# Optimization experiments

Hardware: AMD Instinct MI355X
Metric: run time of the kernel (lower is better)

## Reference

```python
import jax, jax.numpy as jnp
import numpy as np

N_NODES = 50000
N_EDGES = 800000
H = 128            # node_hidden_size
T = 2              # num_prop_rounds


def setup_inputs() -> dict:
    key = jax.random.key(0)
    ks = jax.random.split(key, 10)
    hv = jax.random.normal(ks[0], (N_NODES, H), dtype=jnp.float32)
    he = jax.random.normal(ks[1], (N_EDGES, 1), dtype=jnp.float32)
    src = jax.random.randint(ks[2], (N_EDGES,), 0, N_NODES, dtype=jnp.int32)
    dst = jax.random.randint(ks[3], (N_EDGES,), 0, N_NODES, dtype=jnp.int32)
    # per-round params, stacked on leading T axis; small scale to avoid gate saturation
    W_msg = jax.random.normal(ks[4], (T, 2 * H, 2 * H + 1), dtype=jnp.float32) * 0.05
    b_msg = jax.random.normal(ks[5], (T, 2 * H), dtype=jnp.float32) * 0.05
    W_ih = jax.random.normal(ks[6], (T, 3 * H, 2 * H), dtype=jnp.float32) * 0.05
    W_hh = jax.random.normal(ks[7], (T, 3 * H, H), dtype=jnp.float32) * 0.05
    b_ih = jax.random.normal(ks[8], (T, 3 * H), dtype=jnp.float32) * 0.05
    b_hh = jax.random.normal(ks[9], (T, 3 * H), dtype=jnp.float32) * 0.05
    return dict(hv=hv, he=he, src=src, dst=dst, W_msg=W_msg, b_msg=b_msg,
                W_ih=W_ih, W_hh=W_hh, b_ih=b_ih, b_hh=b_hh)


def _gru_cell(x, h, W_ih, W_hh, b_ih, b_hh):
    # torch.nn.GRUCell math
    gi = x @ W_ih.T + b_ih          # [N, 3H]
    gh = h @ W_hh.T + b_hh          # [N, 3H]
    i_r, i_z, i_n = jnp.split(gi, 3, axis=1)
    h_r, h_z, h_n = jnp.split(gh, 3, axis=1)
    r = jax.nn.sigmoid(i_r + h_r)
    z = jax.nn.sigmoid(i_z + h_z)
    n = jnp.tanh(i_n + r * h_n)
    return (1.0 - z) * n + z * h


def reference(hv, he, src, dst, W_msg, b_msg, W_ih, W_hh, b_ih, b_hh):
    n_nodes = hv.shape[0]
    for t in range(T):
        # per-edge message input: concat([hv_dst, hv_src, he])  [E, 2H+1]
        msg_in = jnp.concatenate([hv[dst], hv[src], he], axis=1)
        edge_act = msg_in @ W_msg[t].T + b_msg[t]          # [E, 2H]
        # ragged sum-reduce over incoming edges (deg-0 nodes get zeros)
        a = jax.ops.segment_sum(edge_act, dst, num_segments=n_nodes)  # [N, 2H]
        hv = _gru_cell(a, hv, W_ih[t], W_hh[t], b_ih[t], b_hh[t])
    return hv
```

## Files before the change

kernel.cpp:

```cpp
#include <hip/hip_runtime.h>
#include <cstdint>
#include <cstddef>

#define N_NODES 50000
#define N_EDGES 800000
#define HDIM 128
#define TROUNDS 2
#define NTILES 3125
#define PACK_PER_T (416 * 64)
#define MAXDEG 64

typedef __attribute__((ext_vector_type(8))) _Float16 half8v;
typedef __attribute__((ext_vector_type(2))) _Float16 half2v;
typedef __attribute__((ext_vector_type(4))) float f32x4;
typedef unsigned short ushort_t;

#define GLD_LDS(gp, lp)                                                        \
  __builtin_amdgcn_global_load_lds(                                            \
      (__attribute__((address_space(1))) const void*)(gp),                     \
      (__attribute__((address_space(3))) void*)(lp), 16, 0, 0)

static __device__ __forceinline__ float sigmoidf_(float x) {
  return 1.0f / (1.0f + __expf(-x));
}
static __device__ __forceinline__ float tanhf_(float x) {
  float xc = fminf(15.0f, fmaxf(-15.0f, x));
  float a = __expf(2.0f * xc);
  return (a - 1.0f) / (a + 1.0f);
}
static __device__ __forceinline__ float f16bits2f(uint32_t hb) {
  ushort_t u = (ushort_t)hb;
  _Float16 h;
  __builtin_memcpy(&h, &u, 2);
  return (float)h;
}

__global__ void pack_all(const float* __restrict__ Wmsg, const float* __restrict__ Wih,
                         const float* __restrict__ Whh, _Float16* __restrict__ W1p,
                         _Float16* __restrict__ W2p, float* __restrict__ we) {
  int g = blockIdx.x * blockDim.x + threadIdx.x;
  if (g < TROUNDS * 256) {
    int t = g >> 8, j = g & 255;
    we[g] = Wmsg[((size_t)t * 256 + j) * 257 + 256];
  }
  if (g >= TROUNDS * PACK_PER_T) return;
  int t = g / PACK_PER_T;
  int r = g % PACK_PER_T;
  int lane = r & 63;
  int fr = r >> 6;
  const float* srcp;
  _Float16* dstp;
  if (fr < 128) {
    int jt = fr >> 3, kt = fr & 7;
    int j = jt * 16 + (lane & 15);
    int k = kt * 32 + ((lane >> 4) << 3);
    srcp = Wmsg + (size_t)t * 256 * 257 + (size_t)j * 257 + k;
    dstp = W1p + ((size_t)t * 128 + fr) * 512 + lane * 8;
  } else {
    int fr2 = fr - 128;
    int chunk = fr2 / 12, idx = fr2 % 12;
    int jt = chunk / 3, pp = chunk % 3;
    int j = pp * 128 + jt * 16 + (lane & 15);
    int k;
    if (idx < 8) {
      k = idx * 32 + ((lane >> 4) << 3);
      srcp = Wih + (size_t)t * 384 * 256 + (size_t)j * 256 + k;
    } else {
      k = (idx - 8) * 32 + ((lane >> 4) << 3);
      srcp = Whh + (size_t)t * 384 * 128 + (size_t)j * 128 + k;
    }
    dstp = W2p + ((size_t)t * 288 + fr2) * 512 + lane * 8;
  }
  #pragma unroll
  for (int e = 0; e < 8; ++e) dstp[e] = (_Float16)srcp[e];
}

__global__ void cast_hv(const float* __restrict__ hv, _Float16* __restrict__ hvh) {
  int i = blockIdx.x * blockDim.x + threadIdx.x;
  if (i >= N_NODES * HDIM / 4) return;
  float4 v = reinterpret_cast<const float4*>(hv)[i];
  half2v o0, o1;
  o0[0] = (_Float16)v.x; o0[1] = (_Float16)v.y;
  o1[0] = (_Float16)v.z; o1[1] = (_Float16)v.w;
  reinterpret_cast<half2v*>(hvh)[i * 2] = o0;
  reinterpret_cast<half2v*>(hvh)[i * 2 + 1] = o1;
}

__global__ void fill_pad(const int* __restrict__ src, const int* __restrict__ dst,
                         const float* __restrict__ he, int* __restrict__ cnt,
                         uint32_t* __restrict__ csr) {
  int e = blockIdx.x * blockDim.x + threadIdx.x;
  if (e >= N_EDGES) return;
  int d = dst[e];
  int slot = atomicAdd(&cnt[d], 1);
  if (slot < MAXDEG) {
    _Float16 hh = (_Float16)he[e];
    ushort_t hb;
    __builtin_memcpy(&hb, &hh, 2);
    uint32_t en = ((uint32_t)hb << 16) | (uint32_t)src[e];
    csr[(size_t)d * MAXDEG + slot] = en;
  }
}

__global__ void gather_h(const _Float16* __restrict__ hvh, const int* __restrict__ cnt,
                         const uint32_t* __restrict__ csr, _Float16* __restrict__ S_h,
                         float* __restrict__ hsum, float* __restrict__ deg_f, int n) {
  int wid = (int)((blockIdx.x * blockDim.x + threadIdx.x) >> 6);
  int lane = threadIdx.x & 63;
  if (wid >= n) return;
  int deg = min(cnt[wid], MAXDEG);
  uint32_t ent = (lane < deg) ? csr[(size_t)wid * MAXDEG + lane] : 0u;
  float a0 = 0.f, a1 = 0.f, hs = 0.f;
  int k = 0;
  for (; k + 3 < deg; k += 4) {
    uint32_t e0 = __shfl(ent, k), e1 = __shfl(ent, k + 1);
    uint32_t e2 = __shfl(ent, k + 2), e3 = __shfl(ent, k + 3);
    half2v v0 = *reinterpret_cast<const half2v*>(hvh + (size_t)(e0 & 0xffffu) * HDIM + lane * 2);
    half2v v1 = *reinterpret_cast<const half2v*>(hvh + (size_t)(e1 & 0xffffu) * HDIM + lane * 2);
    half2v v2 = *reinterpret_cast<const half2v*>(hvh + (size_t)(e2 & 0xffffu) * HDIM + lane * 2);
    half2v v3 = *reinterpret_cast<const half2v*>(hvh + (size_t)(e3 & 0xffffu) * HDIM + lane * 2);
    a0 += ((float)v0[0] + (float)v1[0]) + ((float)v2[0] + (float)v3[0]);
    a1 += ((float)v0[1] + (float)v1[1]) + ((float)v2[1] + (float)v3[1]);
    hs += (f16bits2f(e0 >> 16) + f16bits2f(e1 >> 16)) +
          (f16bits2f(e2 >> 16) + f16bits2f(e3 >> 16));
  }
  for (; k < deg; ++k) {
    uint32_t e0 = __shfl(ent, k);
    half2v v0 = *reinterpret_cast<const half2v*>(hvh + (size_t)(e0 & 0xffffu) * HDIM + lane * 2);
    a0 += (float)v0[0];
    a1 += (float)v0[1];
    hs += f16bits2f(e0 >> 16);
  }
  half2v o;
  o[0] = (_Float16)a0;
  o[1] = (_Float16)a1;
  *reinterpret_cast<half2v*>(S_h + (size_t)wid * HDIM + lane * 2) = o;
  if (lane == 0) hsum[wid] = hs;
  if (lane == 1) deg_f[wid] = (float)deg;
}

__global__ __launch_bounds__(256, 4) void u1_kernel(
    const float* __restrict__ hv, const _Float16* __restrict__ S_h,
    const float* __restrict__ deg_f, const float* __restrict__ hsum,
    const _Float16* __restrict__ W1p, const float* __restrict__ we,
    const float* __restrict__ bmsg, _Float16* __restrict__ a_out) {
  __shared__ _Float16 buf[2][8 * 512];
  const int tid = threadIdx.x;
  const int wv = tid >> 6, lane = tid & 63;
  const int tile = blockIdx.x * 4 + wv;
  const bool act = (tile < NTILES);
  const int rowA = tile * 16 + (lane & 15);
  const int koff = (lane >> 4) * 8;
  const int m0 = (lane >> 4) * 4;

  {
    const _Float16* g = W1p + (size_t)(wv * 2) * 512 + lane * 8;
    #pragma unroll
    for (int i = 0; i < 2; ++i) GLD_LDS(g + i * 512, &buf[0][(wv * 2 + i) * 512]);
  }

  half8v x[8];
  float degs[4], hss[4];
  if (act) {
    float deg = deg_f[rowA];
    const float* hrow = hv + (size_t)rowA * HDIM;
    #pragma unroll
    for (int kt = 0; kt < 4; ++kt) {
      const float* sp = hrow + kt * 32 + koff;
      #pragma unroll
      for (int e = 0; e < 8; ++e) x[kt][e] = (_Float16)(sp[e] * deg);
    }
    const _Float16* srow = S_h + (size_t)rowA * HDIM + koff;
    #pragma unroll
    for (int kt = 0; kt < 4; ++kt)
      x[4 + kt] = *reinterpret_cast<const half8v*>(srow + kt * 32);
    #pragma unroll
    for (int rr = 0; rr < 4; ++rr) {
      degs[rr] = deg_f[tile * 16 + m0 + rr];
      hss[rr] = hsum[tile * 16 + m0 + rr];
    }
  }

  #pragma unroll 1
  for (int jt = 0; jt < 16; ++jt) {
    __syncthreads();
    if (jt < 15) {
      const _Float16* g = W1p + (size_t)(jt + 1) * 4096 + (size_t)(wv * 2) * 512 + lane * 8;
      #pragma unroll
      for (int i = 0; i < 2; ++i) GLD_LDS(g + i * 512, &buf[(jt + 1) & 1][(wv * 2 + i) * 512]);
    }
    const _Float16* B = &buf[jt & 1][0];
    f32x4 acc = {0.f, 0.f, 0.f, 0.f};
    #pragma unroll
    for (int kt = 0; kt < 8; ++kt) {
      half8v b = *reinterpret_cast<const half8v*>(B + (size_t)kt * 512 + lane * 8);
      acc = __builtin_amdgcn_mfma_f32_16x16x32_f16(x[kt], b, acc, 0, 0, 0);
    }
    if (act) {
      int j = jt * 16 + (lane & 15);
      float bm = bmsg[j], w = we[j];
      #pragma unroll
      for (int rr = 0; rr < 4; ++rr)
        a_out[(size_t)(tile * 16 + m0 + rr) * 256 + j] =
            (_Float16)(acc[rr] + degs[rr] * bm + hss[rr] * w);
    }
  }
}

__global__ __launch_bounds__(256, 4) void u2_kernel(
    const float* __restrict__ hv_in, const _Float16* __restrict__ a_in,
    const _Float16* __restrict__ W2p, const float* __restrict__ bih,
    const float* __restrict__ bhh, float* __restrict__ hv_out,
    _Float16* __restrict__ hvh_out) {
  __shared__ _Float16 buf[2][12 * 512];
  const int tid = threadIdx.x;
  const int wv = tid >> 6, lane = tid & 63;
  const int tile = blockIdx.x * 4 + wv;
  const bool act = (tile < NTILES);
  const int rowA = tile * 16 + (lane & 15);
  const int koff = (lane >> 4) * 8;
  const int m0 = (lane >> 4) * 4;

  auto stage = [&](int n) {
    const _Float16* g = W2p + (size_t)n * 6144 + (size_t)(wv * 3) * 512 + lane * 8;
    _Float16* l = &buf[n & 1][(wv * 3) * 512];
    #pragma unroll
    for (int i = 0; i < 3; ++i) GLD_LDS(g + i * 512, l + i * 512);
  };

  stage(0);

  half8v a8[8], h4[4];
  if (act) {
    const _Float16* ar = a_in + (size_t)rowA * 256 + koff;
    #pragma unroll
    for (int kt = 0; kt < 8; ++kt)
      a8[kt] = *reinterpret_cast<const half8v*>(ar + kt * 32);
    const float* hr = hv_in + (size_t)rowA * HDIM + koff;
    #pragma unroll
    for (int kt = 0; kt < 4; ++kt) {
      #pragma unroll
      for (int e = 0; e < 8; ++e) h4[kt][e] = (_Float16)hr[kt * 32 + e];
    }
  }

  auto compute = [&](const _Float16* B, f32x4& ai, f32x4& ag) {
    ai = (f32x4){0.f, 0.f, 0.f, 0.f};
    ag = (f32x4){0.f, 0.f, 0.f, 0.f};
    #pragma unroll
    for (int kt = 0; kt < 8; ++kt) {
      half8v b = *reinterpret_cast<const half8v*>(B + (size_t)kt * 512 + lane * 8);
      ai = __builtin_amdgcn_mfma_f32_16x16x32_f16(a8[kt], b, ai, 0, 0, 0);
    }
    #pragma unroll
    for (int kt = 0; kt < 4; ++kt) {
      half8v b = *reinterpret_cast<const half8v*>(B + (size_t)(8 + kt) * 512 + lane * 8);
      ag = __builtin_amdgcn_mfma_f32_16x16x32_f16(h4[kt], b, ag, 0, 0, 0);
    }
  };

  f32x4 rreg, zreg, ai, ag;
  #pragma unroll 1
  for (int jt = 0; jt < 8; ++jt) {
    const int c0 = jt * 3;
    const int fcol = jt * 16 + (lane & 15);
    __syncthreads();
    stage(c0 + 1);
    compute(&buf[c0 & 1][0], ai, ag);
    if (act) {
      float bi = bih[fcol], bq = bhh[fcol];
      #pragma unroll
      for (int rr = 0; rr < 4; ++rr) rreg[rr] = sigmoidf_(ai[rr] + bi + ag[rr] + bq);
    }
    __syncthreads();
    stage(c0 + 2);
    compute(&buf[(c0 + 1) & 1][0], ai, ag);
    if (act) {
      float bi = bih[128 + fcol], bq = bhh[128 + fcol];
      #pragma unroll
      for (int rr = 0; rr < 4; ++rr) zreg[rr] = sigmoidf_(ai[rr] + bi + ag[rr] + bq);
    }
    __syncthreads();
    if (jt < 7) stage(c0 + 3);
    compute(&buf[(c0 + 2) & 1][0], ai, ag);
    if (act) {
      float bi = bih[256 + fcol], bq = bhh[256 + fcol];
      #pragma unroll
      for (int rr = 0; rr < 4; ++rr) {
        int node = tile * 16 + m0 + rr;
        float n = tanhf_(ai[rr] + bi + rreg[rr] * (ag[rr] + bq));
        float h = hv_in[(size_t)node * HDIM + fcol];
        float hn = (1.f - zreg[rr]) * n + zreg[rr] * h;
        hv_out[(size_t)node * HDIM + fcol] = hn;
        hvh_out[(size_t)node * HDIM + fcol] = (_Float16)hn;
      }
    }
  }
}

extern "C" void kernel_launch(void* const* d_in, const int* in_sizes, int n_in,
                              void* d_out, int out_size, void* d_ws, size_t ws_size,
                              hipStream_t stream) {
  const float* hv   = (const float*)d_in[0];
  const float* he   = (const float*)d_in[1];
  const int*   src  = (const int*)d_in[2];
  const int*   dst  = (const int*)d_in[3];
  const float* Wmsg = (const float*)d_in[4];
  const float* bmsg = (const float*)d_in[5];
  const float* Wih  = (const float*)d_in[6];
  const float* Whh  = (const float*)d_in[7];
  const float* bih  = (const float*)d_in[8];
  const float* bhh  = (const float*)d_in[9];

  char* p = (char*)d_ws;
  auto alloc = [&](size_t bytes) { char* r = p; p += (bytes + 255) & ~(size_t)255; return r; };
  _Float16* S_h   = (_Float16*)alloc((size_t)N_NODES * HDIM * 2);
  _Float16* a_buf = (_Float16*)alloc((size_t)N_NODES * 256 * 2);
  _Float16* hvh   = (_Float16*)alloc((size_t)N_NODES * HDIM * 2);
  float*    deg_f = (float*)alloc((size_t)N_NODES * 4);
  float*    hsum  = (float*)alloc((size_t)N_NODES * 4);
  float*    we    = (float*)alloc((size_t)TROUNDS * 256 * 4);
  const size_t W1PT = (size_t)128 * 512;
  const size_t W2PT = (size_t)288 * 512;
  _Float16* W1p = (_Float16*)alloc(TROUNDS * W1PT * 2);
  _Float16* W2p = (_Float16*)alloc(TROUNDS * W2PT * 2);
  int*      cnt = (int*)alloc((size_t)N_NODES * 4);
  uint32_t* csr = (uint32_t*)alloc((size_t)N_NODES * MAXDEG * 4);

  hipMemsetAsync(cnt, 0, (size_t)N_NODES * 4, stream);

  pack_all<<<(TROUNDS * PACK_PER_T + 255) / 256, 256, 0, stream>>>(Wmsg, Wih, Whh, W1p, W2p, we);
  cast_hv<<<(N_NODES * HDIM / 4 + 255) / 256, 256, 0, stream>>>(hv, hvh);
  fill_pad<<<(N_EDGES + 255) / 256, 256, 0, stream>>>(src, dst, he, cnt, csr);

  const float* hcur = hv;
  float* outp = (float*)d_out;
  const int ugrid = (NTILES + 3) / 4;
  for (int t = 0; t < TROUNDS; ++t) {
    gather_h<<<(N_NODES + 3) / 4, 256, 0, stream>>>(hvh, cnt, csr, S_h, hsum, deg_f, N_NODES);
    u1_kernel<<<ugrid, 256, 0, stream>>>(
        hcur, S_h, deg_f, hsum, W1p + (size_t)t * W1PT,
        we + (size_t)t * 256, bmsg + (size_t)t * 256, a_buf);
    u2_kernel<<<ugrid, 256, 0, stream>>>(
        hcur, a_buf, W2p + (size_t)t * W2PT,
        bih + (size_t)t * 384, bhh + (size_t)t * 384, outp, hvh);
    hcur = outp;
  }
  (void)in_sizes; (void)n_in; (void)out_size; (void)ws_size;
}
```

Baseline: 242.6 us.

## Process two row tiles per wave and use 512-thread blocks in GRU/message GEMMs

Each wave now computes two 16-row tiles against the same LDS-staged weight fragment, so every B operand read from LDS feeds two MFMAs. Blocks grow to 8 waves covering 16 tiles, which amortizes the weight staging per block over four times as many rows and cuts the grid size. In exchange, register pressure roughly doubles for the A fragments and accumulators, and there are fewer blocks (about 196) to spread across the CUs, which may reduce occupancy and load balance.

```diff
diff --git a/kernel.cpp b/kernel.cpp
--- a/kernel.cpp
+++ b/kernel.cpp
@@ -139,7 +139,7 @@
   if (lane == 1) deg_f[wid] = (float)deg;
 }
 
-__global__ __launch_bounds__(256, 4) void u1_kernel(
+__global__ __launch_bounds__(512, 2) void u1_kernel(
     const float* __restrict__ hv, const _Float16* __restrict__ S_h,
     const float* __restrict__ deg_f, const float* __restrict__ hsum,
     const _Float16* __restrict__ W1p, const float* __restrict__ we,
@@ -147,67 +147,77 @@
   __shared__ _Float16 buf[2][8 * 512];
   const int tid = threadIdx.x;
   const int wv = tid >> 6, lane = tid & 63;
-  const int tile = blockIdx.x * 4 + wv;
-  const bool act = (tile < NTILES);
-  const int rowA = tile * 16 + (lane & 15);
+  const int tile0 = blockIdx.x * 16 + wv * 2;
+  const int tile1 = tile0 + 1;
+  const bool act0 = (tile0 < NTILES), act1 = (tile1 < NTILES);
   const int koff = (lane >> 4) * 8;
   const int m0 = (lane >> 4) * 4;
 
-  {
-    const _Float16* g = W1p + (size_t)(wv * 2) * 512 + lane * 8;
-    #pragma unroll
-    for (int i = 0; i < 2; ++i) GLD_LDS(g + i * 512, &buf[0][(wv * 2 + i) * 512]);
-  }
-
-  half8v x[8];
-  float degs[4], hss[4];
-  if (act) {
-    float deg = deg_f[rowA];
-    const float* hrow = hv + (size_t)rowA * HDIM;
-    #pragma unroll
-    for (int kt = 0; kt < 4; ++kt) {
-      const float* sp = hrow + kt * 32 + koff;
-      #pragma unroll
-      for (int e = 0; e < 8; ++e) x[kt][e] = (_Float16)(sp[e] * deg);
-    }
-    const _Float16* srow = S_h + (size_t)rowA * HDIM + koff;
-    #pragma unroll
-    for (int kt = 0; kt < 4; ++kt)
-      x[4 + kt] = *reinterpret_cast<const half8v*>(srow + kt * 32);
-    #pragma unroll
-    for (int rr = 0; rr < 4; ++rr) {
-      degs[rr] = deg_f[tile * 16 + m0 + rr];
-      hss[rr] = hsum[tile * 16 + m0 + rr];
+  auto stage1 = [&](int c) {
+    const _Float16* g = W1p + (size_t)c * 4096 + wv * 512 + lane * 8;
+    GLD_LDS(g, &buf[c & 1][wv * 512]);
+  };
+  stage1(0);
+
+  half8v x0[8], x1[8];
+  float degs[2][4], hss[2][4];
+  #pragma unroll
+  for (int tt = 0; tt < 2; ++tt) {
+    const int tile = tt ? tile1 : tile0;
+    const bool act = tt ? act1 : act0;
+    half8v* x = tt ? x1 : x0;
+    if (act) {
+      int rowA = tile * 16 + (lane & 15);
+      float deg = deg_f[rowA];
+      const float* hrow = hv + (size_t)rowA * HDIM;
+      #pragma unroll
+      for (int kt = 0; kt < 4; ++kt) {
+        const float* sp = hrow + kt * 32 + koff;
+        #pragma unroll
+        for (int e = 0; e < 8; ++e) x[kt][e] = (_Float16)(sp[e] * deg);
+      }
+      const _Float16* srow = S_h + (size_t)rowA * HDIM + koff;
+      #pragma unroll
+      for (int kt = 0; kt < 4; ++kt)
+        x[4 + kt] = *reinterpret_cast<const half8v*>(srow + kt * 32);
+      #pragma unroll
+      for (int rr = 0; rr < 4; ++rr) {
+        degs[tt][rr] = deg_f[tile * 16 + m0 + rr];
+        hss[tt][rr] = hsum[tile * 16 + m0 + rr];
+      }
     }
   }
 
   #pragma unroll 1
   for (int jt = 0; jt < 16; ++jt) {
     __syncthreads();
-    if (jt < 15) {
-      const _Float16* g = W1p + (size_t)(jt + 1) * 4096 + (size_t)(wv * 2) * 512 + lane * 8;
-      #pragma unroll
-      for (int i = 0; i < 2; ++i) GLD_LDS(g + i * 512, &buf[(jt + 1) & 1][(wv * 2 + i) * 512]);
-    }
+    if (jt < 15) stage1(jt + 1);
     const _Float16* B = &buf[jt & 1][0];
-    f32x4 acc = {0.f, 0.f, 0.f, 0.f};
+    f32x4 acc0 = {0.f, 0.f, 0.f, 0.f}, acc1 = {0.f, 0.f, 0.f, 0.f};
     #pragma unroll
     for (int kt = 0; kt < 8; ++kt) {
       half8v b = *reinterpret_cast<const half8v*>(B + (size_t)kt * 512 + lane * 8);
-      acc = __builtin_amdgcn_mfma_f32_16x16x32_f16(x[kt], b, acc, 0, 0, 0);
-    }
-    if (act) {
-      int j = jt * 16 + (lane & 15);
-      float bm = bmsg[j], w = we[j];
+      acc0 = __builtin_amdgcn_mfma_f32_16x16x32_f16(x0[kt], b, acc0, 0, 0, 0);
+      acc1 = __builtin_amdgcn_mfma_f32_16x16x32_f16(x1[kt], b, acc1, 0, 0, 0);
+    }
+    int j = jt * 16 + (lane & 15);
+    float bm = bmsg[j], w = we[j];
+    if (act0) {
       #pragma unroll
       for (int rr = 0; rr < 4; ++rr)
-        a_out[(size_t)(tile * 16 + m0 + rr) * 256 + j] =
-            (_Float16)(acc[rr] + degs[rr] * bm + hss[rr] * w);
-    }
-  }
-}
-
-__global__ __launch_bounds__(256, 4) void u2_kernel(
+        a_out[(size_t)(tile0 * 16 + m0 + rr) * 256 + j] =
+            (_Float16)(acc0[rr] + degs[0][rr] * bm + hss[0][rr] * w);
+    }
+    if (act1) {
+      #pragma unroll
+      for (int rr = 0; rr < 4; ++rr)
+        a_out[(size_t)(tile1 * 16 + m0 + rr) * 256 + j] =
+            (_Float16)(acc1[rr] + degs[1][rr] * bm + hss[1][rr] * w);
+    }
+  }
+}
+
+__global__ __launch_bounds__(512, 2) void u2_kernel(
     const float* __restrict__ hv_in, const _Float16* __restrict__ a_in,
     const _Float16* __restrict__ W2p, const float* __restrict__ bih,
     const float* __restrict__ bhh, float* __restrict__ hv_out,
@@ -215,84 +225,116 @@
   __shared__ _Float16 buf[2][12 * 512];
   const int tid = threadIdx.x;
   const int wv = tid >> 6, lane = tid & 63;
-  const int tile = blockIdx.x * 4 + wv;
-  const bool act = (tile < NTILES);
-  const int rowA = tile * 16 + (lane & 15);
+  const int tile0 = blockIdx.x * 16 + wv * 2;
+  const int tile1 = tile0 + 1;
+  const bool act0 = (tile0 < NTILES), act1 = (tile1 < NTILES);
   const int koff = (lane >> 4) * 8;
   const int m0 = (lane >> 4) * 4;
 
-  auto stage = [&](int n) {
-    const _Float16* g = W2p + (size_t)n * 6144 + (size_t)(wv * 3) * 512 + lane * 8;
-    _Float16* l = &buf[n & 1][(wv * 3) * 512];
-    #pragma unroll
-    for (int i = 0; i < 3; ++i) GLD_LDS(g + i * 512, l + i * 512);
+  auto stage = [&](int c) {
+    const _Float16* g = W2p + (size_t)c * 6144 + wv * 512 + lane * 8;
+    GLD_LDS(g, &buf[c & 1][wv * 512]);
+    if (wv < 4) {
+      const _Float16* g2 = W2p + (size_t)c * 6144 + (8 + wv) * 512 + lane * 8;
+      GLD_LDS(g2, &buf[c & 1][(8 + wv) * 512]);
+    }
   };
-
   stage(0);
 
-  half8v a8[8], h4[4];
-  if (act) {
-    const _Float16* ar = a_in + (size_t)rowA * 256 + koff;
-    #pragma unroll
-    for (int kt = 0; kt < 8; ++kt)
-      a8[kt] = *reinterpret_cast<const half8v*>(ar + kt * 32);
-    const float* hr = hv_in + (size_t)rowA * HDIM + koff;
-    #pragma unroll
-    for (int kt = 0; kt < 4; ++kt) {
-      #pragma unroll
-      for (int e = 0; e < 8; ++e) h4[kt][e] = (_Float16)hr[kt * 32 + e];
-    }
-  }
-
-  auto compute = [&](const _Float16* B, f32x4& ai, f32x4& ag) {
-    ai = (f32x4){0.f, 0.f, 0.f, 0.f};
-    ag = (f32x4){0.f, 0.f, 0.f, 0.f};
+  half8v a80[8], a81[8], h40[4], h41[4];
+  #pragma unroll
+  for (int tt = 0; tt < 2; ++tt) {
+    const int tile = tt ? tile1 : tile0;
+    const bool act = tt ? act1 : act0;
+    half8v* a8 = tt ? a81 : a80;
+    half8v* h4 = tt ? h41 : h40;
+    if (act) {
+      int rowA = tile * 16 + (lane & 15);
+      const _Float16* ar = a_in + (size_t)rowA * 256 + koff;
+      #pragma unroll
+      for (int kt = 0; kt < 8; ++kt)
+        a8[kt] = *reinterpret_cast<const half8v*>(ar + kt * 32);
+      const float* hr = hv_in + (size_t)rowA * HDIM + koff;
+      #pragma unroll
+      for (int kt = 0; kt < 4; ++kt) {
+        #pragma unroll
+        for (int e = 0; e < 8; ++e) h4[kt][e] = (_Float16)hr[kt * 32 + e];
+      }
+    }
+  }
+
+  auto compute = [&](const _Float16* B, f32x4& ai0, f32x4& ag0, f32x4& ai1, f32x4& ag1) {
+    ai0 = (f32x4){0.f, 0.f, 0.f, 0.f};
+    ag0 = (f32x4){0.f, 0.f, 0.f, 0.f};
+    ai1 = (f32x4){0.f, 0.f, 0.f, 0.f};
+    ag1 = (f32x4){0.f, 0.f, 0.f, 0.f};
     #pragma unroll
     for (int kt = 0; kt < 8; ++kt) {
       half8v b = *reinterpret_cast<const half8v*>(B + (size_t)kt * 512 + lane * 8);
-      ai = __builtin_amdgcn_mfma_f32_16x16x32_f16(a8[kt], b, ai, 0, 0, 0);
+      ai0 = __builtin_amdgcn_mfma_f32_16x16x32_f16(a80[kt], b, ai0, 0, 0, 0);
+      ai1 = __builtin_amdgcn_mfma_f32_16x16x32_f16(a81[kt], b, ai1, 0, 0, 0);
     }
     #pragma unroll
     for (int kt = 0; kt < 4; ++kt) {
       half8v b = *reinterpret_cast<const half8v*>(B + (size_t)(8 + kt) * 512 + lane * 8);
-      ag = __builtin_amdgcn_mfma_f32_16x16x32_f16(h4[kt], b, ag, 0, 0, 0);
+      ag0 = __builtin_amdgcn_mfma_f32_16x16x32_f16(h40[kt], b, ag0, 0, 0, 0);
+      ag1 = __builtin_amdgcn_mfma_f32_16x16x32_f16(h41[kt], b, ag1, 0, 0, 0);
     }
   };
 
-  f32x4 rreg, zreg, ai, ag;
+  f32x4 rreg0, rreg1, zreg0, zreg1, ai0, ag0, ai1, ag1;
   #pragma unroll 1
   for (int jt = 0; jt < 8; ++jt) {
     const int c0 = jt * 3;
     const int fcol = jt * 16 + (lane & 15);
     __syncthreads();
     stage(c0 + 1);
-    compute(&buf[c0 & 1][0], ai, ag);
-    if (act) {
+    compute(&buf[c0 & 1][0], ai0, ag0, ai1, ag1);
+    {
       float bi = bih[fcol], bq = bhh[fcol];
       #pragma unroll
-      for (int rr = 0; rr < 4; ++rr) rreg[rr] = sigmoidf_(ai[rr] + bi + ag[rr] + bq);
+      for (int rr = 0; rr < 4; ++rr) {
+        rreg0[rr] = sigmoidf_(ai0[rr] + bi + ag0[rr] + bq);
+        rreg1[rr] = sigmoidf_(ai1[rr] + bi + ag1[rr] + bq);
+      }
     }
     __syncthreads();
     stage(c0 + 2);
-    compute(&buf[(c0 + 1) & 1][0], ai, ag);
-    if (act) {
+    compute(&buf[(c0 + 1) & 1][0], ai0, ag0, ai1, ag1);
+    {
       float bi = bih[128 + fcol], bq = bhh[128 + fcol];
       #pragma unroll
-      for (int rr = 0; rr < 4; ++rr) zreg[rr] = sigmoidf_(ai[rr] + bi + ag[rr] + bq);
+      for (int rr = 0; rr < 4; ++rr) {
+        zreg0[rr] = sigmoidf_(ai0[rr] + bi + ag0[rr] + bq);
+        zreg1[rr] = sigmoidf_(ai1[rr] + bi + ag1[rr] + bq);
+      }
     }
     __syncthreads();
     if (jt < 7) stage(c0 + 3);
-    compute(&buf[(c0 + 2) & 1][0], ai, ag);
-    if (act) {
+    compute(&buf[(c0 + 2) & 1][0], ai0, ag0, ai1, ag1);
+    {
       float bi = bih[256 + fcol], bq = bhh[256 + fcol];
-      #pragma unroll
-      for (int rr = 0; rr < 4; ++rr) {
-        int node = tile * 16 + m0 + rr;
-        float n = tanhf_(ai[rr] + bi + rreg[rr] * (ag[rr] + bq));
-        float h = hv_in[(size_t)node * HDIM + fcol];
-        float hn = (1.f - zreg[rr]) * n + zreg[rr] * h;
-        hv_out[(size_t)node * HDIM + fcol] = hn;
-        hvh_out[(size_t)node * HDIM + fcol] = (_Float16)hn;
+      if (act0) {
+        #pragma unroll
+        for (int rr = 0; rr < 4; ++rr) {
+          int node = tile0 * 16 + m0 + rr;
+          float n = tanhf_(ai0[rr] + bi + rreg0[rr] * (ag0[rr] + bq));
+          float h = hv_in[(size_t)node * HDIM + fcol];
+          float hn = (1.f - zreg0[rr]) * n + zreg0[rr] * h;
+          hv_out[(size_t)node * HDIM + fcol] = hn;
+          hvh_out[(size_t)node * HDIM + fcol] = (_Float16)hn;
+        }
+      }
+      if (act1) {
+        #pragma unroll
+        for (int rr = 0; rr < 4; ++rr) {
+          int node = tile1 * 16 + m0 + rr;
+          float n = tanhf_(ai1[rr] + bi + rreg1[rr] * (ag1[rr] + bq));
+          float h = hv_in[(size_t)node * HDIM + fcol];
+          float hn = (1.f - zreg1[rr]) * n + zreg1[rr] * h;
+          hv_out[(size_t)node * HDIM + fcol] = hn;
+          hvh_out[(size_t)node * HDIM + fcol] = (_Float16)hn;
+        }
       }
     }
   }
@@ -335,13 +377,13 @@
 
   const float* hcur = hv;
   float* outp = (float*)d_out;
-  const int ugrid = (NTILES + 3) / 4;
+  const int ugrid = (NTILES + 15) / 16;
   for (int t = 0; t < TROUNDS; ++t) {
     gather_h<<<(N_NODES + 3) / 4, 256, 0, stream>>>(hvh, cnt, csr, S_h, hsum, deg_f, N_NODES);
-    u1_kernel<<<ugrid, 256, 0, stream>>>(
+    u1_kernel<<<ugrid, 512, 0, stream>>>(
         hcur, S_h, deg_f, hsum, W1p + (size_t)t * W1PT,
         we + (size_t)t * 256, bmsg + (size_t)t * 256, a_buf);
-    u2_kernel<<<ugrid, 256, 0, stream>>>(
+    u2_kernel<<<ugrid, 512, 0, stream>>>(
         hcur, a_buf, W2p + (size_t)t * W2PT,
         bih + (size_t)t * 384, bhh + (size_t)t * 384, outp, hvh);
     hcur = outp;
```

Result: slower. 255.5 us (+5.3%).
